# Kernel optimization log

Hardware: AMD Instinct MI355X
Metric: run time of the kernel (lower is better)

The kernel has to match this reference:

```python
import jax, jax.numpy as jnp
import numpy as np
from jax import lax

T, B, D = 200, 1024, 128  # max_len, batch, units (= input feature dim)


def setup_inputs() -> dict:
    key = jax.random.key(0)
    ks = jax.random.split(key, 16)
    s = 1.0 / np.sqrt(D)
    inp = {
        "inputs": jax.random.normal(ks[0], (T, B, D), dtype=jnp.float32),
        "state": jnp.zeros((B, D), dtype=jnp.float32),
        "att_score": jax.random.uniform(ks[1], (T, B, 1), dtype=jnp.float32),
        # binary validity mask [B, T], float because it multiplies the state
        "mask": (jax.random.uniform(ks[2], (B, T)) < 0.9).astype(jnp.float32),
        "max_len": T,
        # u gate (Bilinear: Dense(a) with bias + Dense(b) no bias)
        "Wau": jax.random.normal(ks[3], (D, D), dtype=jnp.float32) * s,
        "bau": jnp.zeros((D,), dtype=jnp.float32),
        "Wbu": jax.random.normal(ks[4], (D, D), dtype=jnp.float32) * s,
        # r gate
        "War": jax.random.normal(ks[5], (D, D), dtype=jnp.float32) * s,
        "bar": jnp.zeros((D,), dtype=jnp.float32),
        "Wbr": jax.random.normal(ks[6], (D, D), dtype=jnp.float32) * s,
        # candidate memory
        "Wac": jax.random.normal(ks[7], (D, D), dtype=jnp.float32) * s,
        "bac": jnp.zeros((D,), dtype=jnp.float32),
        "Wbc": jax.random.normal(ks[8], (D, D), dtype=jnp.float32) * s,
    }
    return inp


def reference(inputs, state, att_score, mask, max_len,
              Wau, bau, Wbu, War, bar, Wbr, Wac, bac, Wbc):
    # time-major mask [T, B, 1]
    mask_t = jnp.swapaxes(mask, 0, 1)[:, :, None]

    def step(s, xs):
        x, a, m = xs  # x:[B,D], a:[B,1], m:[B,1]
        u = jax.nn.sigmoid(x @ Wau + bau + s @ Wbu)
        r = jax.nn.sigmoid(x @ War + bar + s @ Wbr)
        c = jnp.tanh(x @ Wac + bac + r * (s @ Wbc))
        u_ = a * u
        new = (1.0 - u_) * s + u_ * c
        s = new * m + s * (1.0 - m)
        return s, None

    final_state, _ = lax.scan(step, state, (inputs, att_score, mask_t))
    return final_state
```

## Files before the change

kernel.cpp:

```cpp
#include <hip/hip_runtime.h>
#include <stdint.h>

#define T_LEN 200
#define B_SZ  1024
#define D_DIM 128
#define LOG2E 1.44269504088896340736f

typedef __bf16 bf16_t;
typedef __bf16 bf16x8 __attribute__((ext_vector_type(8)));
typedef float  f32x4  __attribute__((ext_vector_type(4)));

union BF8 { bf16x8 v; bf16_t e[8]; };

__device__ inline float rcp_f(float x) { return __builtin_amdgcn_rcpf(x); }

__device__ inline uint32_t cvt_pk_bf16(float a, float b) {
  uint32_t r;
  asm("v_cvt_pk_bf16_f32 %0, %1, %2" : "=v"(r) : "v"(a), "v"(b));
  return r;
}

#define BAR_LDS() asm volatile("s_waitcnt lgkmcnt(0)\n\ts_barrier" ::: "memory")

__global__ __launch_bounds__(512, 2) void augru_fused(
    const float* __restrict__ x,
    const float* __restrict__ state,
    const float* __restrict__ att,
    const float* __restrict__ mask,
    const float* __restrict__ Wau, const float* __restrict__ bau,
    const float* __restrict__ Wbu,
    const float* __restrict__ War, const float* __restrict__ bar,
    const float* __restrict__ Wbr,
    const float* __restrict__ Wac, const float* __restrict__ bac,
    const float* __restrict__ Wbc,
    float* __restrict__ out)
{
  __shared__ bf16_t xb[2][2048];
  __shared__ bf16_t sb[2][2048];
  __shared__ float  am_lds[(T_LEN + 1) * 16];

  const int tid = threadIdx.x;
  const int w  = tid >> 6;
  const int l  = tid & 63;
  const int lm = l & 15;
  const int lg = l >> 4;
  const int bb = blockIdx.x;
  const int R0 = bb * 16;
  const int col = w * 16 + lm;

  BF8 xu[4], xr[4], xc[4];
  BF8 su[4], sr[4], sc[4];
#pragma unroll
  for (int kk = 0; kk < 4; ++kk) {
#pragma unroll
    for (int j = 0; j < 8; ++j) {
      int k = kk * 32 + lg * 8 + j;
      xu[kk].e[j] = (bf16_t)(Wau[k * 128 + col] * LOG2E);
      xr[kk].e[j] = (bf16_t)(War[k * 128 + col] * LOG2E);
      xc[kk].e[j] = (bf16_t)(Wac[k * 128 + col] * (2.0f * LOG2E));
      su[kk].e[j] = (bf16_t)(Wbu[k * 128 + col] * LOG2E);
      sr[kk].e[j] = (bf16_t)(Wbr[k * 128 + col] * LOG2E);
      sc[kk].e[j] = (bf16_t)(Wbc[k * 128 + col] * (2.0f * LOG2E));
    }
  }
  const float b_u = bau[col] * LOG2E;
  const float b_r = bar[col] * LOG2E;
  const float b_c = bac[col] * (2.0f * LOG2E);

  const f32x4 biasU = {b_u, b_u, b_u, b_u};
  const f32x4 biasR = {b_r, b_r, b_r, b_r};
  const f32x4 biasC = {b_c, b_c, b_c, b_c};
  const f32x4 zero4 = {0.f, 0.f, 0.f, 0.f};

  for (int idx = tid; idx < (T_LEN + 1) * 16; idx += 512) {
    int t = idx >> 4; if (t > T_LEN - 1) t = T_LEN - 1;
    int row = idx & 15;
    am_lds[idx] = rcp_f(att[t * B_SZ + R0 + row] * mask[(R0 + row) * T_LEN + t]);
  }

  float sreg[4];
#pragma unroll
  for (int i = 0; i < 4; ++i)
    sreg[i] = state[(R0 + lg * 4 + i) * 128 + col];

  for (int idx = tid; idx < 2048; idx += 512) {
    int row = idx >> 7, k = idx & 127;
    sb[0][(k >> 3) * 128 + (row ^ (2 * ((k >> 3) & 1))) * 8 + (k & 7)] =
        (bf16_t)state[(R0 + row) * 128 + k];
  }

  const int srow = tid & 15;
  const int sc4  = tid >> 4;
  const int stg_pos = (sc4 >> 1) * 128 + srow * 8 + (sc4 & 1) * 4;
  const float* xrow = x + (size_t)(R0 + srow) * 128 + sc4 * 4;
  const size_t xstep = (size_t)B_SZ * 128;
  const size_t xoff_max = (size_t)(T_LEN - 1) * xstep;

  {
    float4 v0 = *(const float4*)(xrow);
    float4 v1 = *(const float4*)(xrow + xstep);
    uint2 p0, p1;
    p0.x = cvt_pk_bf16(v0.x, v0.y); p0.y = cvt_pk_bf16(v0.z, v0.w);
    p1.x = cvt_pk_bf16(v1.x, v1.y); p1.y = cvt_pk_bf16(v1.z, v1.w);
    *(uint2*)&xb[0][stg_pos] = p0;
    *(uint2*)&xb[1][stg_pos] = p1;
  }
  float4 xqA = *(const float4*)(xrow + 2 * xstep);
  float4 xqB = *(const float4*)(xrow + 3 * xstep);
  size_t offA = 4 * xstep;
  size_t offB = 5 * xstep;

  __syncthreads();

  f32x4 gU, gR, gC;
  {
    bf16x8 ax[4];
#pragma unroll
    for (int kk = 0; kk < 4; ++kk)
      ax[kk] = *(const bf16x8*)&xb[0][kk * 512 + 8 * l];
    gU = __builtin_amdgcn_mfma_f32_16x16x32_bf16(ax[0], xu[0].v, biasU, 0, 0, 0);
    gR = __builtin_amdgcn_mfma_f32_16x16x32_bf16(ax[0], xr[0].v, biasR, 0, 0, 0);
    gC = __builtin_amdgcn_mfma_f32_16x16x32_bf16(ax[0], xc[0].v, biasC, 0, 0, 0);
#pragma unroll
    for (int kk = 1; kk < 4; ++kk) {
      gU = __builtin_amdgcn_mfma_f32_16x16x32_bf16(ax[kk], xu[kk].v, gU, 0, 0, 0);
      gR = __builtin_amdgcn_mfma_f32_16x16x32_bf16(ax[kk], xr[kk].v, gR, 0, 0, 0);
      gC = __builtin_amdgcn_mfma_f32_16x16x32_bf16(ax[kk], xc[kk].v, gC, 0, 0, 0);
    }
  }
  union F4 { float4 v; float e[4]; } amv, amn;
  amv.v = *(const float4*)&am_lds[lg * 4];
  const float* am_ptr = &am_lds[16 + lg * 4];

  const int lx8   = 8 * (l ^ (2 * (lg & 1)));
  const int psi   = 2 * ((col >> 3) & 1);
  const int wbase = (col >> 3) * 128 + lg * 32 + (col & 7);

  BAR_LDS();

  auto step = [&](int t, float4& xq, size_t& xoff) {
    const int rp = t & 1;

    bf16x8 as_[4], ax[4];
#pragma unroll
    for (int kk = 0; kk < 4; ++kk)
      as_[kk] = *(const bf16x8*)&sb[rp][kk * 512 + lx8];
#pragma unroll
    for (int kk = 0; kk < 4; ++kk)
      ax[kk]  = *(const bf16x8*)&xb[rp ^ 1][kk * 512 + 8 * l];

    amn.v = *(const float4*)am_ptr;
    am_ptr += 16;

    {
      uint2 p;
      p.x = cvt_pk_bf16(xq.x, xq.y);
      p.y = cvt_pk_bf16(xq.z, xq.w);
      *(uint2*)&xb[rp][stg_pos] = p;
    }
    xq = *(const float4*)(xrow + xoff);
    xoff += 2 * xstep; if (xoff > xoff_max) xoff = xoff_max;

    f32x4 aU = __builtin_amdgcn_mfma_f32_16x16x32_bf16(as_[0], su[0].v, gU, 0, 0, 0);
    f32x4 aR = __builtin_amdgcn_mfma_f32_16x16x32_bf16(as_[0], sr[0].v, gR, 0, 0, 0);
    f32x4 bC = __builtin_amdgcn_mfma_f32_16x16x32_bf16(as_[0], sc[0].v, zero4, 0, 0, 0);
#pragma unroll
    for (int kk = 1; kk < 4; ++kk) {
      aU = __builtin_amdgcn_mfma_f32_16x16x32_bf16(as_[kk], su[kk].v, aU, 0, 0, 0);
      aR = __builtin_amdgcn_mfma_f32_16x16x32_bf16(as_[kk], sr[kk].v, aR, 0, 0, 0);
      bC = __builtin_amdgcn_mfma_f32_16x16x32_bf16(as_[kk], sc[kk].v, bC, 0, 0, 0);
    }
    f32x4 nU = __builtin_amdgcn_mfma_f32_16x16x32_bf16(ax[0], xu[0].v, biasU, 0, 0, 0);
    f32x4 nR = __builtin_amdgcn_mfma_f32_16x16x32_bf16(ax[0], xr[0].v, biasR, 0, 0, 0);
    f32x4 nC = __builtin_amdgcn_mfma_f32_16x16x32_bf16(ax[0], xc[0].v, biasC, 0, 0, 0);
#pragma unroll
    for (int kk = 1; kk < 4; ++kk) {
      nU = __builtin_amdgcn_mfma_f32_16x16x32_bf16(ax[kk], xu[kk].v, nU, 0, 0, 0);
      nR = __builtin_amdgcn_mfma_f32_16x16x32_bf16(ax[kk], xr[kk].v, nR, 0, 0, 0);
      nC = __builtin_amdgcn_mfma_f32_16x16x32_bf16(ax[kk], xc[kk].v, nC, 0, 0, 0);
    }

    bf16_t* wbuf = sb[rp ^ 1];
#pragma unroll
    for (int i = 0; i < 4; ++i) {
      float Xu = __builtin_amdgcn_exp2f(-aU[i]);
      float k  = rcp_f(fmaf(Xu, amv.e[i], amv.e[i]));
      float r  = rcp_f(1.0f + __builtin_amdgcn_exp2f(-aR[i]));
      float wc = fmaf(r, bC[i], gC[i]);
      float cg = fmaf(-2.0f, rcp_f(__builtin_amdgcn_exp2f(wc) + 1.0f), 1.0f);
      float sf = fmaf(k, cg - sreg[i], sreg[i]);
      sreg[i] = sf;
      wbuf[wbase + 8 * (i ^ psi)] = (bf16_t)sf;
    }

    gU = nU; gR = nR; gC = nC;
    amv.v = amn.v;

    BAR_LDS();
  };

#pragma unroll 1
  for (int t = 0; t < T_LEN; t += 2) {
    step(t,     xqA, offA);
    step(t + 1, xqB, offB);
  }

#pragma unroll
  for (int i = 0; i < 4; ++i)
    out[(R0 + lg * 4 + i) * 128 + col] = sreg[i];
}

extern "C" void kernel_launch(void* const* d_in, const int* in_sizes, int n_in,
                              void* d_out, int out_size, void* d_ws, size_t ws_size,
                              hipStream_t stream)
{
  const float* x    = (const float*)d_in[0];
  const float* st   = (const float*)d_in[1];
  const float* att  = (const float*)d_in[2];
  const float* mask = (const float*)d_in[3];
  const float* Wau  = (const float*)d_in[5];
  const float* bau  = (const float*)d_in[6];
  const float* Wbu  = (const float*)d_in[7];
  const float* War  = (const float*)d_in[8];
  const float* bar  = (const float*)d_in[9];
  const float* Wbr  = (const float*)d_in[10];
  const float* Wac  = (const float*)d_in[11];
  const float* bac  = (const float*)d_in[12];
  const float* Wbc  = (const float*)d_in[13];

  (void)d_ws; (void)ws_size;

  augru_fused<<<dim3(64), dim3(512), 0, stream>>>(
      x, st, att, mask, Wau, bau, Wbu, War, bar, Wbr, Wac, bac, Wbc,
      (float*)d_out);
}
```

Baseline: 293.7 us.

## Halve block to 4 waves, each computing two 16-column tiles

The block shrinks from 8 waves to 4, and each wave now computes two 16-column output tiles. The A-operand fragments loaded from LDS are reused across both tiles, and two independent MFMA accumulator chains are interleaved. Global x staging changes to 8 floats per thread. This aims to cut per-step barrier cost and LDS fragment reads, and to add ILP in the latency-bound recurrence. In exchange, per-wave register pressure roughly doubles and each wave does twice the serial elementwise gate work per step.

```diff
diff --git a/kernel.cpp b/kernel.cpp
--- a/kernel.cpp
+++ b/kernel.cpp
@@ -11,6 +11,7 @@
 typedef float  f32x4  __attribute__((ext_vector_type(4)));
 
 union BF8 { bf16x8 v; bf16_t e[8]; };
+struct F8 { float4 a, b; };
 
 __device__ inline float rcp_f(float x) { return __builtin_amdgcn_rcpf(x); }
 
@@ -22,7 +23,7 @@
 
 #define BAR_LDS() asm volatile("s_waitcnt lgkmcnt(0)\n\ts_barrier" ::: "memory")
 
-__global__ __launch_bounds__(512, 2) void augru_fused(
+__global__ __launch_bounds__(256, 1) void augru_fused(
     const float* __restrict__ x,
     const float* __restrict__ state,
     const float* __restrict__ att,
@@ -46,99 +47,124 @@
   const int lg = l >> 4;
   const int bb = blockIdx.x;
   const int R0 = bb * 16;
-  const int col = w * 16 + lm;
-
-  BF8 xu[4], xr[4], xc[4];
-  BF8 su[4], sr[4], sc[4];
-#pragma unroll
-  for (int kk = 0; kk < 4; ++kk) {
-#pragma unroll
-    for (int j = 0; j < 8; ++j) {
-      int k = kk * 32 + lg * 8 + j;
-      xu[kk].e[j] = (bf16_t)(Wau[k * 128 + col] * LOG2E);
-      xr[kk].e[j] = (bf16_t)(War[k * 128 + col] * LOG2E);
-      xc[kk].e[j] = (bf16_t)(Wac[k * 128 + col] * (2.0f * LOG2E));
-      su[kk].e[j] = (bf16_t)(Wbu[k * 128 + col] * LOG2E);
-      sr[kk].e[j] = (bf16_t)(Wbr[k * 128 + col] * LOG2E);
-      sc[kk].e[j] = (bf16_t)(Wbc[k * 128 + col] * (2.0f * LOG2E));
-    }
-  }
-  const float b_u = bau[col] * LOG2E;
-  const float b_r = bar[col] * LOG2E;
-  const float b_c = bac[col] * (2.0f * LOG2E);
-
-  const f32x4 biasU = {b_u, b_u, b_u, b_u};
-  const f32x4 biasR = {b_r, b_r, b_r, b_r};
-  const f32x4 biasC = {b_c, b_c, b_c, b_c};
+  const int c0 = w * 32 + lm;
+
+  BF8 xu[2][4], xr[2][4], xc[2][4];
+  BF8 su[2][4], sr[2][4], sc[2][4];
+  float b_u[2], b_r[2], b_c[2];
+#pragma unroll
+  for (int tt = 0; tt < 2; ++tt) {
+    const int colt = c0 + tt * 16;
+#pragma unroll
+    for (int kk = 0; kk < 4; ++kk) {
+#pragma unroll
+      for (int j = 0; j < 8; ++j) {
+        int k = kk * 32 + lg * 8 + j;
+        xu[tt][kk].e[j] = (bf16_t)(Wau[k * 128 + colt] * LOG2E);
+        xr[tt][kk].e[j] = (bf16_t)(War[k * 128 + colt] * LOG2E);
+        xc[tt][kk].e[j] = (bf16_t)(Wac[k * 128 + colt] * (2.0f * LOG2E));
+        su[tt][kk].e[j] = (bf16_t)(Wbu[k * 128 + colt] * LOG2E);
+        sr[tt][kk].e[j] = (bf16_t)(Wbr[k * 128 + colt] * LOG2E);
+        sc[tt][kk].e[j] = (bf16_t)(Wbc[k * 128 + colt] * (2.0f * LOG2E));
+      }
+    }
+    b_u[tt] = bau[colt] * LOG2E;
+    b_r[tt] = bar[colt] * LOG2E;
+    b_c[tt] = bac[colt] * (2.0f * LOG2E);
+  }
+  const f32x4 biasU[2] = {{b_u[0], b_u[0], b_u[0], b_u[0]},
+                          {b_u[1], b_u[1], b_u[1], b_u[1]}};
+  const f32x4 biasR[2] = {{b_r[0], b_r[0], b_r[0], b_r[0]},
+                          {b_r[1], b_r[1], b_r[1], b_r[1]}};
+  const f32x4 biasC[2] = {{b_c[0], b_c[0], b_c[0], b_c[0]},
+                          {b_c[1], b_c[1], b_c[1], b_c[1]}};
   const f32x4 zero4 = {0.f, 0.f, 0.f, 0.f};
 
-  for (int idx = tid; idx < (T_LEN + 1) * 16; idx += 512) {
+  for (int idx = tid; idx < (T_LEN + 1) * 16; idx += 256) {
     int t = idx >> 4; if (t > T_LEN - 1) t = T_LEN - 1;
     int row = idx & 15;
     am_lds[idx] = rcp_f(att[t * B_SZ + R0 + row] * mask[(R0 + row) * T_LEN + t]);
   }
 
-  float sreg[4];
-#pragma unroll
-  for (int i = 0; i < 4; ++i)
-    sreg[i] = state[(R0 + lg * 4 + i) * 128 + col];
-
-  for (int idx = tid; idx < 2048; idx += 512) {
+  float sreg[2][4];
+#pragma unroll
+  for (int tt = 0; tt < 2; ++tt)
+#pragma unroll
+    for (int i = 0; i < 4; ++i)
+      sreg[tt][i] = state[(R0 + lg * 4 + i) * 128 + c0 + tt * 16];
+
+  for (int idx = tid; idx < 2048; idx += 256) {
     int row = idx >> 7, k = idx & 127;
     sb[0][(k >> 3) * 128 + (row ^ (2 * ((k >> 3) & 1))) * 8 + (k & 7)] =
         (bf16_t)state[(R0 + row) * 128 + k];
   }
 
   const int srow = tid & 15;
-  const int sc4  = tid >> 4;
-  const int stg_pos = (sc4 >> 1) * 128 + srow * 8 + (sc4 & 1) * 4;
-  const float* xrow = x + (size_t)(R0 + srow) * 128 + sc4 * 4;
+  const int sc8  = tid >> 4;
+  const int stg_pos = sc8 * 128 + srow * 8;
+  const float* xrow = x + (size_t)(R0 + srow) * 128 + sc8 * 8;
   const size_t xstep = (size_t)B_SZ * 128;
   const size_t xoff_max = (size_t)(T_LEN - 1) * xstep;
 
+  auto ldf8 = [&](size_t off) {
+    F8 q;
+    q.a = *(const float4*)(xrow + off);
+    q.b = *(const float4*)(xrow + off + 4);
+    return q;
+  };
+  auto stage = [&](int buf, const F8& q) {
+    uint4 p;
+    p.x = cvt_pk_bf16(q.a.x, q.a.y);
+    p.y = cvt_pk_bf16(q.a.z, q.a.w);
+    p.z = cvt_pk_bf16(q.b.x, q.b.y);
+    p.w = cvt_pk_bf16(q.b.z, q.b.w);
+    *(uint4*)&xb[buf][stg_pos] = p;
+  };
+
   {
-    float4 v0 = *(const float4*)(xrow);
-    float4 v1 = *(const float4*)(xrow + xstep);
-    uint2 p0, p1;
-    p0.x = cvt_pk_bf16(v0.x, v0.y); p0.y = cvt_pk_bf16(v0.z, v0.w);
-    p1.x = cvt_pk_bf16(v1.x, v1.y); p1.y = cvt_pk_bf16(v1.z, v1.w);
-    *(uint2*)&xb[0][stg_pos] = p0;
-    *(uint2*)&xb[1][stg_pos] = p1;
-  }
-  float4 xqA = *(const float4*)(xrow + 2 * xstep);
-  float4 xqB = *(const float4*)(xrow + 3 * xstep);
+    F8 q0 = ldf8(0), q1 = ldf8(xstep);
+    stage(0, q0);
+    stage(1, q1);
+  }
+  F8 xqA = ldf8(2 * xstep);
+  F8 xqB = ldf8(3 * xstep);
   size_t offA = 4 * xstep;
   size_t offB = 5 * xstep;
 
   __syncthreads();
 
-  f32x4 gU, gR, gC;
+  f32x4 gU[2], gR[2], gC[2];
   {
     bf16x8 ax[4];
 #pragma unroll
     for (int kk = 0; kk < 4; ++kk)
       ax[kk] = *(const bf16x8*)&xb[0][kk * 512 + 8 * l];
-    gU = __builtin_amdgcn_mfma_f32_16x16x32_bf16(ax[0], xu[0].v, biasU, 0, 0, 0);
-    gR = __builtin_amdgcn_mfma_f32_16x16x32_bf16(ax[0], xr[0].v, biasR, 0, 0, 0);
-    gC = __builtin_amdgcn_mfma_f32_16x16x32_bf16(ax[0], xc[0].v, biasC, 0, 0, 0);
-#pragma unroll
-    for (int kk = 1; kk < 4; ++kk) {
-      gU = __builtin_amdgcn_mfma_f32_16x16x32_bf16(ax[kk], xu[kk].v, gU, 0, 0, 0);
-      gR = __builtin_amdgcn_mfma_f32_16x16x32_bf16(ax[kk], xr[kk].v, gR, 0, 0, 0);
-      gC = __builtin_amdgcn_mfma_f32_16x16x32_bf16(ax[kk], xc[kk].v, gC, 0, 0, 0);
-    }
+#pragma unroll
+    for (int tt = 0; tt < 2; ++tt) {
+      gU[tt] = __builtin_amdgcn_mfma_f32_16x16x32_bf16(ax[0], xu[tt][0].v, biasU[tt], 0, 0, 0);
+      gR[tt] = __builtin_amdgcn_mfma_f32_16x16x32_bf16(ax[0], xr[tt][0].v, biasR[tt], 0, 0, 0);
+      gC[tt] = __builtin_amdgcn_mfma_f32_16x16x32_bf16(ax[0], xc[tt][0].v, biasC[tt], 0, 0, 0);
+    }
+#pragma unroll
+    for (int kk = 1; kk < 4; ++kk)
+#pragma unroll
+      for (int tt = 0; tt < 2; ++tt) {
+        gU[tt] = __builtin_amdgcn_mfma_f32_16x16x32_bf16(ax[kk], xu[tt][kk].v, gU[tt], 0, 0, 0);
+        gR[tt] = __builtin_amdgcn_mfma_f32_16x16x32_bf16(ax[kk], xr[tt][kk].v, gR[tt], 0, 0, 0);
+        gC[tt] = __builtin_amdgcn_mfma_f32_16x16x32_bf16(ax[kk], xc[tt][kk].v, gC[tt], 0, 0, 0);
+      }
   }
   union F4 { float4 v; float e[4]; } amv, amn;
   amv.v = *(const float4*)&am_lds[lg * 4];
   const float* am_ptr = &am_lds[16 + lg * 4];
 
   const int lx8   = 8 * (l ^ (2 * (lg & 1)));
-  const int psi   = 2 * ((col >> 3) & 1);
-  const int wbase = (col >> 3) * 128 + lg * 32 + (col & 7);
+  const int psi   = 2 * ((c0 >> 3) & 1);
+  const int wbase = (c0 >> 3) * 128 + lg * 32 + (c0 & 7);
 
   BAR_LDS();
 
-  auto step = [&](int t, float4& xq, size_t& xoff) {
+  auto step = [&](int t, F8& xq, size_t& xoff) {
     const int rp = t & 1;
 
     bf16x8 as_[4], ax[4];
@@ -152,48 +178,62 @@
     amn.v = *(const float4*)am_ptr;
     am_ptr += 16;
 
-    {
-      uint2 p;
-      p.x = cvt_pk_bf16(xq.x, xq.y);
-      p.y = cvt_pk_bf16(xq.z, xq.w);
-      *(uint2*)&xb[rp][stg_pos] = p;
-    }
-    xq = *(const float4*)(xrow + xoff);
+    stage(rp, xq);
+    xq = ldf8(xoff);
     xoff += 2 * xstep; if (xoff > xoff_max) xoff = xoff_max;
 
-    f32x4 aU = __builtin_amdgcn_mfma_f32_16x16x32_bf16(as_[0], su[0].v, gU, 0, 0, 0);
-    f32x4 aR = __builtin_amdgcn_mfma_f32_16x16x32_bf16(as_[0], sr[0].v, gR, 0, 0, 0);
-    f32x4 bC = __builtin_amdgcn_mfma_f32_16x16x32_bf16(as_[0], sc[0].v, zero4, 0, 0, 0);
-#pragma unroll
-    for (int kk = 1; kk < 4; ++kk) {
-      aU = __builtin_amdgcn_mfma_f32_16x16x32_bf16(as_[kk], su[kk].v, aU, 0, 0, 0);
-      aR = __builtin_amdgcn_mfma_f32_16x16x32_bf16(as_[kk], sr[kk].v, aR, 0, 0, 0);
-      bC = __builtin_amdgcn_mfma_f32_16x16x32_bf16(as_[kk], sc[kk].v, bC, 0, 0, 0);
-    }
-    f32x4 nU = __builtin_amdgcn_mfma_f32_16x16x32_bf16(ax[0], xu[0].v, biasU, 0, 0, 0);
-    f32x4 nR = __builtin_amdgcn_mfma_f32_16x16x32_bf16(ax[0], xr[0].v, biasR, 0, 0, 0);
-    f32x4 nC = __builtin_amdgcn_mfma_f32_16x16x32_bf16(ax[0], xc[0].v, biasC, 0, 0, 0);
-#pragma unroll
-    for (int kk = 1; kk < 4; ++kk) {
-      nU = __builtin_amdgcn_mfma_f32_16x16x32_bf16(ax[kk], xu[kk].v, nU, 0, 0, 0);
-      nR = __builtin_amdgcn_mfma_f32_16x16x32_bf16(ax[kk], xr[kk].v, nR, 0, 0, 0);
-      nC = __builtin_amdgcn_mfma_f32_16x16x32_bf16(ax[kk], xc[kk].v, nC, 0, 0, 0);
-    }
+    f32x4 aU[2], aR[2], bC[2];
+#pragma unroll
+    for (int tt = 0; tt < 2; ++tt) {
+      aU[tt] = __builtin_amdgcn_mfma_f32_16x16x32_bf16(as_[0], su[tt][0].v, gU[tt], 0, 0, 0);
+      aR[tt] = __builtin_amdgcn_mfma_f32_16x16x32_bf16(as_[0], sr[tt][0].v, gR[tt], 0, 0, 0);
+      bC[tt] = __builtin_amdgcn_mfma_f32_16x16x32_bf16(as_[0], sc[tt][0].v, zero4, 0, 0, 0);
+    }
+#pragma unroll
+    for (int kk = 1; kk < 4; ++kk)
+#pragma unroll
+      for (int tt = 0; tt < 2; ++tt) {
+        aU[tt] = __builtin_amdgcn_mfma_f32_16x16x32_bf16(as_[kk], su[tt][kk].v, aU[tt], 0, 0, 0);
+        aR[tt] = __builtin_amdgcn_mfma_f32_16x16x32_bf16(as_[kk], sr[tt][kk].v, aR[tt], 0, 0, 0);
+        bC[tt] = __builtin_amdgcn_mfma_f32_16x16x32_bf16(as_[kk], sc[tt][kk].v, bC[tt], 0, 0, 0);
+      }
+    f32x4 nU[2], nR[2], nC[2];
+#pragma unroll
+    for (int tt = 0; tt < 2; ++tt) {
+      nU[tt] = __builtin_amdgcn_mfma_f32_16x16x32_bf16(ax[0], xu[tt][0].v, biasU[tt], 0, 0, 0);
+      nR[tt] = __builtin_amdgcn_mfma_f32_16x16x32_bf16(ax[0], xr[tt][0].v, biasR[tt], 0, 0, 0);
+      nC[tt] = __builtin_amdgcn_mfma_f32_16x16x32_bf16(ax[0], xc[tt][0].v, biasC[tt], 0, 0, 0);
+    }
+#pragma unroll
+    for (int kk = 1; kk < 4; ++kk)
+#pragma unroll
+      for (int tt = 0; tt < 2; ++tt) {
+        nU[tt] = __builtin_amdgcn_mfma_f32_16x16x32_bf16(ax[kk], xu[tt][kk].v, nU[tt], 0, 0, 0);
+        nR[tt] = __builtin_amdgcn_mfma_f32_16x16x32_bf16(ax[kk], xr[tt][kk].v, nR[tt], 0, 0, 0);
+        nC[tt] = __builtin_amdgcn_mfma_f32_16x16x32_bf16(ax[kk], xc[tt][kk].v, nC[tt], 0, 0, 0);
+      }
 
     bf16_t* wbuf = sb[rp ^ 1];
 #pragma unroll
-    for (int i = 0; i < 4; ++i) {
-      float Xu = __builtin_amdgcn_exp2f(-aU[i]);
-      float k  = rcp_f(fmaf(Xu, amv.e[i], amv.e[i]));
-      float r  = rcp_f(1.0f + __builtin_amdgcn_exp2f(-aR[i]));
-      float wc = fmaf(r, bC[i], gC[i]);
-      float cg = fmaf(-2.0f, rcp_f(__builtin_amdgcn_exp2f(wc) + 1.0f), 1.0f);
-      float sf = fmaf(k, cg - sreg[i], sreg[i]);
-      sreg[i] = sf;
-      wbuf[wbase + 8 * (i ^ psi)] = (bf16_t)sf;
-    }
-
-    gU = nU; gR = nR; gC = nC;
+    for (int tt = 0; tt < 2; ++tt) {
+      const int wb = wbase + tt * 256;
+#pragma unroll
+      for (int i = 0; i < 4; ++i) {
+        float Xu = __builtin_amdgcn_exp2f(-aU[tt][i]);
+        float k  = rcp_f(fmaf(Xu, amv.e[i], amv.e[i]));
+        float r  = rcp_f(1.0f + __builtin_amdgcn_exp2f(-aR[tt][i]));
+        float wc = fmaf(r, bC[tt][i], gC[tt][i]);
+        float cg = fmaf(-2.0f, rcp_f(__builtin_amdgcn_exp2f(wc) + 1.0f), 1.0f);
+        float sf = fmaf(k, cg - sreg[tt][i], sreg[tt][i]);
+        sreg[tt][i] = sf;
+        wbuf[wb + 8 * (i ^ psi)] = (bf16_t)sf;
+      }
+    }
+
+#pragma unroll
+    for (int tt = 0; tt < 2; ++tt) {
+      gU[tt] = nU[tt]; gR[tt] = nR[tt]; gC[tt] = nC[tt];
+    }
     amv.v = amn.v;
 
     BAR_LDS();
@@ -206,8 +246,10 @@
   }
 
 #pragma unroll
-  for (int i = 0; i < 4; ++i)
-    out[(R0 + lg * 4 + i) * 128 + col] = sreg[i];
+  for (int tt = 0; tt < 2; ++tt)
+#pragma unroll
+    for (int i = 0; i < 4; ++i)
+      out[(R0 + lg * 4 + i) * 128 + c0 + tt * 16] = sreg[tt][i];
 }
 
 extern "C" void kernel_launch(void* const* d_in, const int* in_sizes, int n_in,
@@ -230,7 +272,7 @@
 
   (void)d_ws; (void)ws_size;
 
-  augru_fused<<<dim3(64), dim3(512), 0, stream>>>(
+  augru_fused<<<dim3(64), dim3(256), 0, stream>>>(
       x, st, att, mask, Wau, bau, Wbu, War, bar, Wbr, Wac, bac, Wbc,
       (float*)d_out);
 }
```

Measured after the change: 338.2 us. 1.15x slower.

## Process two independent 16-row batch tiles per block to interleave recurrences

Applied to the files above, without the earlier changes.

Each block now handles 32 batch rows as two independent 16-row tiles, so the grid shrinks from 64 to 32 blocks. The MFMA chains and gate math of the two tiles are interleaved within each timestep. The goal is to hide MFMA dependency latency and amortize the per-step barrier over twice the work. In exchange it uses half as many CUs, raises register and LDS pressure, and may serialize more work per block.

```diff
diff --git a/kernel.cpp b/kernel.cpp
--- a/kernel.cpp
+++ b/kernel.cpp
@@ -35,9 +35,9 @@
     const float* __restrict__ Wbc,
     float* __restrict__ out)
 {
-  __shared__ bf16_t xb[2][2048];
-  __shared__ bf16_t sb[2][2048];
-  __shared__ float  am_lds[(T_LEN + 1) * 16];
+  __shared__ bf16_t xb[2][2][2048];
+  __shared__ bf16_t sb[2][2][2048];
+  __shared__ float  am_lds[2][T_LEN * 16];
 
   const int tid = threadIdx.x;
   const int w  = tid >> 6;
@@ -45,7 +45,8 @@
   const int lm = l & 15;
   const int lg = l >> 4;
   const int bb = blockIdx.x;
-  const int R0 = bb * 16;
+  const int R0a = bb * 32;
+  const int R0b = bb * 32 + 16;
   const int col = w * 16 + lm;
 
   BF8 xu[4], xr[4], xc[4];
@@ -66,148 +67,202 @@
   const float b_u = bau[col] * LOG2E;
   const float b_r = bar[col] * LOG2E;
   const float b_c = bac[col] * (2.0f * LOG2E);
-
   const f32x4 biasU = {b_u, b_u, b_u, b_u};
   const f32x4 biasR = {b_r, b_r, b_r, b_r};
   const f32x4 biasC = {b_c, b_c, b_c, b_c};
   const f32x4 zero4 = {0.f, 0.f, 0.f, 0.f};
 
-  for (int idx = tid; idx < (T_LEN + 1) * 16; idx += 512) {
-    int t = idx >> 4; if (t > T_LEN - 1) t = T_LEN - 1;
-    int row = idx & 15;
-    am_lds[idx] = rcp_f(att[t * B_SZ + R0 + row] * mask[(R0 + row) * T_LEN + t]);
-  }
-
-  float sreg[4];
-#pragma unroll
-  for (int i = 0; i < 4; ++i)
-    sreg[i] = state[(R0 + lg * 4 + i) * 128 + col];
-
-  for (int idx = tid; idx < 2048; idx += 512) {
-    int row = idx >> 7, k = idx & 127;
-    sb[0][(k >> 3) * 128 + (row ^ (2 * ((k >> 3) & 1))) * 8 + (k & 7)] =
-        (bf16_t)state[(R0 + row) * 128 + k];
+  for (int idx = tid; idx < 2 * T_LEN * 16; idx += 512) {
+    int tile = (idx >= T_LEN * 16);
+    int j = idx - tile * (T_LEN * 16);
+    int t = j >> 4, row = j & 15;
+    int Rb = tile ? R0b : R0a;
+    am_lds[tile][j] = rcp_f(att[t * B_SZ + Rb + row] * mask[(Rb + row) * T_LEN + t]);
+  }
+
+  float sregA[4], sregB[4];
+#pragma unroll
+  for (int i = 0; i < 4; ++i) {
+    sregA[i] = state[(R0a + lg * 4 + i) * 128 + col];
+    sregB[i] = state[(R0b + lg * 4 + i) * 128 + col];
+  }
+
+  for (int idx = tid; idx < 4096; idx += 512) {
+    int tile = idx >> 11, j = idx & 2047;
+    int row = j >> 7, k = j & 127;
+    int Rb = tile ? R0b : R0a;
+    sb[tile][0][(k >> 3) * 128 + (row ^ (2 * ((k >> 3) & 1))) * 8 + (k & 7)] =
+        (bf16_t)state[(Rb + row) * 128 + k];
   }
 
   const int srow = tid & 15;
   const int sc4  = tid >> 4;
   const int stg_pos = (sc4 >> 1) * 128 + srow * 8 + (sc4 & 1) * 4;
-  const float* xrow = x + (size_t)(R0 + srow) * 128 + sc4 * 4;
+  const float* xrowA = x + (size_t)(R0a + srow) * 128 + sc4 * 4;
+  const float* xrowB = x + (size_t)(R0b + srow) * 128 + sc4 * 4;
   const size_t xstep = (size_t)B_SZ * 128;
   const size_t xoff_max = (size_t)(T_LEN - 1) * xstep;
 
   {
-    float4 v0 = *(const float4*)(xrow);
-    float4 v1 = *(const float4*)(xrow + xstep);
-    uint2 p0, p1;
-    p0.x = cvt_pk_bf16(v0.x, v0.y); p0.y = cvt_pk_bf16(v0.z, v0.w);
-    p1.x = cvt_pk_bf16(v1.x, v1.y); p1.y = cvt_pk_bf16(v1.z, v1.w);
-    *(uint2*)&xb[0][stg_pos] = p0;
-    *(uint2*)&xb[1][stg_pos] = p1;
-  }
-  float4 xqA = *(const float4*)(xrow + 2 * xstep);
-  float4 xqB = *(const float4*)(xrow + 3 * xstep);
-  size_t offA = 4 * xstep;
-  size_t offB = 5 * xstep;
+    float4 v;
+    uint2 p;
+    v = *(const float4*)(xrowA);
+    p.x = cvt_pk_bf16(v.x, v.y); p.y = cvt_pk_bf16(v.z, v.w);
+    *(uint2*)&xb[0][0][stg_pos] = p;
+    v = *(const float4*)(xrowA + xstep);
+    p.x = cvt_pk_bf16(v.x, v.y); p.y = cvt_pk_bf16(v.z, v.w);
+    *(uint2*)&xb[0][1][stg_pos] = p;
+    v = *(const float4*)(xrowB);
+    p.x = cvt_pk_bf16(v.x, v.y); p.y = cvt_pk_bf16(v.z, v.w);
+    *(uint2*)&xb[1][0][stg_pos] = p;
+    v = *(const float4*)(xrowB + xstep);
+    p.x = cvt_pk_bf16(v.x, v.y); p.y = cvt_pk_bf16(v.z, v.w);
+    *(uint2*)&xb[1][1][stg_pos] = p;
+  }
+  float4 xqEa = *(const float4*)(xrowA + 2 * xstep);
+  float4 xqEb = *(const float4*)(xrowB + 2 * xstep);
+  float4 xqOa = *(const float4*)(xrowA + 3 * xstep);
+  float4 xqOb = *(const float4*)(xrowB + 3 * xstep);
+  size_t offE = 4 * xstep;
+  size_t offO = 5 * xstep;
 
   __syncthreads();
 
-  f32x4 gU, gR, gC;
+  f32x4 gUa, gRa, gCa, gUb, gRb, gCb;
   {
-    bf16x8 ax[4];
-#pragma unroll
-    for (int kk = 0; kk < 4; ++kk)
-      ax[kk] = *(const bf16x8*)&xb[0][kk * 512 + 8 * l];
-    gU = __builtin_amdgcn_mfma_f32_16x16x32_bf16(ax[0], xu[0].v, biasU, 0, 0, 0);
-    gR = __builtin_amdgcn_mfma_f32_16x16x32_bf16(ax[0], xr[0].v, biasR, 0, 0, 0);
-    gC = __builtin_amdgcn_mfma_f32_16x16x32_bf16(ax[0], xc[0].v, biasC, 0, 0, 0);
+    bf16x8 axA[4], axB[4];
+#pragma unroll
+    for (int kk = 0; kk < 4; ++kk) {
+      axA[kk] = *(const bf16x8*)&xb[0][0][kk * 512 + 8 * l];
+      axB[kk] = *(const bf16x8*)&xb[1][0][kk * 512 + 8 * l];
+    }
+    gUa = __builtin_amdgcn_mfma_f32_16x16x32_bf16(axA[0], xu[0].v, biasU, 0, 0, 0);
+    gRa = __builtin_amdgcn_mfma_f32_16x16x32_bf16(axA[0], xr[0].v, biasR, 0, 0, 0);
+    gCa = __builtin_amdgcn_mfma_f32_16x16x32_bf16(axA[0], xc[0].v, biasC, 0, 0, 0);
+    gUb = __builtin_amdgcn_mfma_f32_16x16x32_bf16(axB[0], xu[0].v, biasU, 0, 0, 0);
+    gRb = __builtin_amdgcn_mfma_f32_16x16x32_bf16(axB[0], xr[0].v, biasR, 0, 0, 0);
+    gCb = __builtin_amdgcn_mfma_f32_16x16x32_bf16(axB[0], xc[0].v, biasC, 0, 0, 0);
 #pragma unroll
     for (int kk = 1; kk < 4; ++kk) {
-      gU = __builtin_amdgcn_mfma_f32_16x16x32_bf16(ax[kk], xu[kk].v, gU, 0, 0, 0);
-      gR = __builtin_amdgcn_mfma_f32_16x16x32_bf16(ax[kk], xr[kk].v, gR, 0, 0, 0);
-      gC = __builtin_amdgcn_mfma_f32_16x16x32_bf16(ax[kk], xc[kk].v, gC, 0, 0, 0);
-    }
-  }
-  union F4 { float4 v; float e[4]; } amv, amn;
-  amv.v = *(const float4*)&am_lds[lg * 4];
-  const float* am_ptr = &am_lds[16 + lg * 4];
+      gUa = __builtin_amdgcn_mfma_f32_16x16x32_bf16(axA[kk], xu[kk].v, gUa, 0, 0, 0);
+      gRa = __builtin_amdgcn_mfma_f32_16x16x32_bf16(axA[kk], xr[kk].v, gRa, 0, 0, 0);
+      gCa = __builtin_amdgcn_mfma_f32_16x16x32_bf16(axA[kk], xc[kk].v, gCa, 0, 0, 0);
+      gUb = __builtin_amdgcn_mfma_f32_16x16x32_bf16(axB[kk], xu[kk].v, gUb, 0, 0, 0);
+      gRb = __builtin_amdgcn_mfma_f32_16x16x32_bf16(axB[kk], xr[kk].v, gRb, 0, 0, 0);
+      gCb = __builtin_amdgcn_mfma_f32_16x16x32_bf16(axB[kk], xc[kk].v, gCb, 0, 0, 0);
+    }
+  }
 
   const int lx8   = 8 * (l ^ (2 * (lg & 1)));
   const int psi   = 2 * ((col >> 3) & 1);
   const int wbase = (col >> 3) * 128 + lg * 32 + (col & 7);
+  int am_off = lg * 4;
 
   BAR_LDS();
 
-  auto step = [&](int t, float4& xq, size_t& xoff) {
+  auto step = [&](int t, float4& xqa, float4& xqb, size_t& xoff) {
     const int rp = t & 1;
 
-    bf16x8 as_[4], ax[4];
-#pragma unroll
-    for (int kk = 0; kk < 4; ++kk)
-      as_[kk] = *(const bf16x8*)&sb[rp][kk * 512 + lx8];
-#pragma unroll
-    for (int kk = 0; kk < 4; ++kk)
-      ax[kk]  = *(const bf16x8*)&xb[rp ^ 1][kk * 512 + 8 * l];
-
-    amn.v = *(const float4*)am_ptr;
-    am_ptr += 16;
+    bf16x8 asA[4], asB[4];
+#pragma unroll
+    for (int kk = 0; kk < 4; ++kk) {
+      asA[kk] = *(const bf16x8*)&sb[0][rp][kk * 512 + lx8];
+      asB[kk] = *(const bf16x8*)&sb[1][rp][kk * 512 + lx8];
+    }
+    union F4 { float4 v; float e[4]; } amA, amB;
+    amA.v = *(const float4*)&am_lds[0][am_off];
+    amB.v = *(const float4*)&am_lds[1][am_off];
+    am_off += 16;
 
     {
       uint2 p;
-      p.x = cvt_pk_bf16(xq.x, xq.y);
-      p.y = cvt_pk_bf16(xq.z, xq.w);
-      *(uint2*)&xb[rp][stg_pos] = p;
-    }
-    xq = *(const float4*)(xrow + xoff);
+      p.x = cvt_pk_bf16(xqa.x, xqa.y); p.y = cvt_pk_bf16(xqa.z, xqa.w);
+      *(uint2*)&xb[0][rp][stg_pos] = p;
+      p.x = cvt_pk_bf16(xqb.x, xqb.y); p.y = cvt_pk_bf16(xqb.z, xqb.w);
+      *(uint2*)&xb[1][rp][stg_pos] = p;
+    }
+    xqa = *(const float4*)(xrowA + xoff);
+    xqb = *(const float4*)(xrowB + xoff);
     xoff += 2 * xstep; if (xoff > xoff_max) xoff = xoff_max;
 
-    f32x4 aU = __builtin_amdgcn_mfma_f32_16x16x32_bf16(as_[0], su[0].v, gU, 0, 0, 0);
-    f32x4 aR = __builtin_amdgcn_mfma_f32_16x16x32_bf16(as_[0], sr[0].v, gR, 0, 0, 0);
-    f32x4 bC = __builtin_amdgcn_mfma_f32_16x16x32_bf16(as_[0], sc[0].v, zero4, 0, 0, 0);
+    f32x4 aRa = __builtin_amdgcn_mfma_f32_16x16x32_bf16(asA[0], sr[0].v, gRa, 0, 0, 0);
+    f32x4 aRb = __builtin_amdgcn_mfma_f32_16x16x32_bf16(asB[0], sr[0].v, gRb, 0, 0, 0);
+    f32x4 bCa = __builtin_amdgcn_mfma_f32_16x16x32_bf16(asA[0], sc[0].v, zero4, 0, 0, 0);
+    f32x4 bCb = __builtin_amdgcn_mfma_f32_16x16x32_bf16(asB[0], sc[0].v, zero4, 0, 0, 0);
+    f32x4 aUa = __builtin_amdgcn_mfma_f32_16x16x32_bf16(asA[0], su[0].v, gUa, 0, 0, 0);
+    f32x4 aUb = __builtin_amdgcn_mfma_f32_16x16x32_bf16(asB[0], su[0].v, gUb, 0, 0, 0);
 #pragma unroll
     for (int kk = 1; kk < 4; ++kk) {
-      aU = __builtin_amdgcn_mfma_f32_16x16x32_bf16(as_[kk], su[kk].v, aU, 0, 0, 0);
-      aR = __builtin_amdgcn_mfma_f32_16x16x32_bf16(as_[kk], sr[kk].v, aR, 0, 0, 0);
-      bC = __builtin_amdgcn_mfma_f32_16x16x32_bf16(as_[kk], sc[kk].v, bC, 0, 0, 0);
-    }
-    f32x4 nU = __builtin_amdgcn_mfma_f32_16x16x32_bf16(ax[0], xu[0].v, biasU, 0, 0, 0);
-    f32x4 nR = __builtin_amdgcn_mfma_f32_16x16x32_bf16(ax[0], xr[0].v, biasR, 0, 0, 0);
-    f32x4 nC = __builtin_amdgcn_mfma_f32_16x16x32_bf16(ax[0], xc[0].v, biasC, 0, 0, 0);
+      aRa = __builtin_amdgcn_mfma_f32_16x16x32_bf16(asA[kk], sr[kk].v, aRa, 0, 0, 0);
+      aRb = __builtin_amdgcn_mfma_f32_16x16x32_bf16(asB[kk], sr[kk].v, aRb, 0, 0, 0);
+      bCa = __builtin_amdgcn_mfma_f32_16x16x32_bf16(asA[kk], sc[kk].v, bCa, 0, 0, 0);
+      bCb = __builtin_amdgcn_mfma_f32_16x16x32_bf16(asB[kk], sc[kk].v, bCb, 0, 0, 0);
+      aUa = __builtin_amdgcn_mfma_f32_16x16x32_bf16(asA[kk], su[kk].v, aUa, 0, 0, 0);
+      aUb = __builtin_amdgcn_mfma_f32_16x16x32_bf16(asB[kk], su[kk].v, aUb, 0, 0, 0);
+    }
+
+    bf16x8 axA[4], axB[4];
+#pragma unroll
+    for (int kk = 0; kk < 4; ++kk) {
+      axA[kk] = *(const bf16x8*)&xb[0][rp ^ 1][kk * 512 + 8 * l];
+      axB[kk] = *(const bf16x8*)&xb[1][rp ^ 1][kk * 512 + 8 * l];
+    }
+    f32x4 nUa = __builtin_amdgcn_mfma_f32_16x16x32_bf16(axA[0], xu[0].v, biasU, 0, 0, 0);
+    f32x4 nUb = __builtin_amdgcn_mfma_f32_16x16x32_bf16(axB[0], xu[0].v, biasU, 0, 0, 0);
+    f32x4 nRa = __builtin_amdgcn_mfma_f32_16x16x32_bf16(axA[0], xr[0].v, biasR, 0, 0, 0);
+    f32x4 nRb = __builtin_amdgcn_mfma_f32_16x16x32_bf16(axB[0], xr[0].v, biasR, 0, 0, 0);
+    f32x4 nCa = __builtin_amdgcn_mfma_f32_16x16x32_bf16(axA[0], xc[0].v, biasC, 0, 0, 0);
+    f32x4 nCb = __builtin_amdgcn_mfma_f32_16x16x32_bf16(axB[0], xc[0].v, biasC, 0, 0, 0);
 #pragma unroll
     for (int kk = 1; kk < 4; ++kk) {
-      nU = __builtin_amdgcn_mfma_f32_16x16x32_bf16(ax[kk], xu[kk].v, nU, 0, 0, 0);
-      nR = __builtin_amdgcn_mfma_f32_16x16x32_bf16(ax[kk], xr[kk].v, nR, 0, 0, 0);
-      nC = __builtin_amdgcn_mfma_f32_16x16x32_bf16(ax[kk], xc[kk].v, nC, 0, 0, 0);
-    }
-
-    bf16_t* wbuf = sb[rp ^ 1];
+      nUa = __builtin_amdgcn_mfma_f32_16x16x32_bf16(axA[kk], xu[kk].v, nUa, 0, 0, 0);
+      nUb = __builtin_amdgcn_mfma_f32_16x16x32_bf16(axB[kk], xu[kk].v, nUb, 0, 0, 0);
+      nRa = __builtin_amdgcn_mfma_f32_16x16x32_bf16(axA[kk], xr[kk].v, nRa, 0, 0, 0);
+      nRb = __builtin_amdgcn_mfma_f32_16x16x32_bf16(axB[kk], xr[kk].v, nRb, 0, 0, 0);
+      nCa = __builtin_amdgcn_mfma_f32_16x16x32_bf16(axA[kk], xc[kk].v, nCa, 0, 0, 0);
+      nCb = __builtin_amdgcn_mfma_f32_16x16x32_bf16(axB[kk], xc[kk].v, nCb, 0, 0, 0);
+    }
+
+    bf16_t* wbA = sb[0][rp ^ 1];
+    bf16_t* wbB = sb[1][rp ^ 1];
 #pragma unroll
     for (int i = 0; i < 4; ++i) {
-      float Xu = __builtin_amdgcn_exp2f(-aU[i]);
-      float k  = rcp_f(fmaf(Xu, amv.e[i], amv.e[i]));
-      float r  = rcp_f(1.0f + __builtin_amdgcn_exp2f(-aR[i]));
-      float wc = fmaf(r, bC[i], gC[i]);
-      float cg = fmaf(-2.0f, rcp_f(__builtin_amdgcn_exp2f(wc) + 1.0f), 1.0f);
-      float sf = fmaf(k, cg - sreg[i], sreg[i]);
-      sreg[i] = sf;
-      wbuf[wbase + 8 * (i ^ psi)] = (bf16_t)sf;
-    }
-
-    gU = nU; gR = nR; gC = nC;
-    amv.v = amn.v;
+      float XuA = __builtin_amdgcn_exp2f(-aUa[i]);
+      float kA  = rcp_f(fmaf(XuA, amA.e[i], amA.e[i]));
+      float rA  = rcp_f(1.0f + __builtin_amdgcn_exp2f(-aRa[i]));
+      float wcA = fmaf(rA, bCa[i], gCa[i]);
+      float cgA = fmaf(-2.0f, rcp_f(__builtin_amdgcn_exp2f(wcA) + 1.0f), 1.0f);
+      float sfA = fmaf(kA, cgA - sregA[i], sregA[i]);
+      sregA[i] = sfA;
+      wbA[wbase + 8 * (i ^ psi)] = (bf16_t)sfA;
+
+      float XuB = __builtin_amdgcn_exp2f(-aUb[i]);
+      float kB  = rcp_f(fmaf(XuB, amB.e[i], amB.e[i]));
+      float rB  = rcp_f(1.0f + __builtin_amdgcn_exp2f(-aRb[i]));
+      float wcB = fmaf(rB, bCb[i], gCb[i]);
+      float cgB = fmaf(-2.0f, rcp_f(__builtin_amdgcn_exp2f(wcB) + 1.0f), 1.0f);
+      float sfB = fmaf(kB, cgB - sregB[i], sregB[i]);
+      sregB[i] = sfB;
+      wbB[wbase + 8 * (i ^ psi)] = (bf16_t)sfB;
+    }
+
+    gUa = nUa; gRa = nRa; gCa = nCa;
+    gUb = nUb; gRb = nRb; gCb = nCb;
 
     BAR_LDS();
   };
 
 #pragma unroll 1
   for (int t = 0; t < T_LEN; t += 2) {
-    step(t,     xqA, offA);
-    step(t + 1, xqB, offB);
-  }
-
-#pragma unroll
-  for (int i = 0; i < 4; ++i)
-    out[(R0 + lg * 4 + i) * 128 + col] = sreg[i];
+    step(t,     xqEa, xqEb, offE);
+    step(t + 1, xqOa, xqOb, offO);
+  }
+
+#pragma unroll
+  for (int i = 0; i < 4; ++i) {
+    out[(R0a + lg * 4 + i) * 128 + col] = sregA[i];
+    out[(R0b + lg * 4 + i) * 128 + col] = sregB[i];
+  }
 }
 
 extern "C" void kernel_launch(void* const* d_in, const int* in_sizes, int n_in,
@@ -230,7 +285,7 @@
 
   (void)d_ws; (void)ws_size;
 
-  augru_fused<<<dim3(64), dim3(512), 0, stream>>>(
+  augru_fused<<<dim3(32), dim3(512), 0, stream>>>(
       x, st, att, mask, Wau, bau, Wbu, War, bar, Wbr, Wac, bac, Wbc,
       (float*)d_out);
 }
```

Result: slower. 408.3 us (+39.0%).
